# Kernel optimization log

Hardware: AMD Instinct MI355X
Metric: run time of the kernel (lower is better)

The kernel has to match this reference:

```python
import jax, jax.numpy as jnp
import numpy as np

B, L, D = 4, 2048, 64
N_HEAD = 4
LOCALITY = 0.2
PI = 3.141592653589793


def setup_inputs() -> dict:
    key = jax.random.key(0)
    k1, k2, k3 = jax.random.split(key, 3)
    mesh = jax.random.uniform(k1, (B, L, 2), dtype=jnp.float32)
    inputs = jax.random.normal(k2, (B, L, D), dtype=jnp.float32)
    lmda = jax.random.uniform(k3, (N_HEAD, 1, 1), dtype=jnp.float32)
    return {"mesh": mesh, "inputs": inputs, "lmda": lmda}


def reference(mesh, inputs, lmda):
    FMAX = jnp.finfo(jnp.float32).max
    # pairwise squared distances: (B, L, L)
    diff = mesh[:, :, None, :] - mesh[:, None, :, :]
    m_dist = jnp.sum(diff * diff, axis=-1)
    # per-head scale in (0, inf): tan(pi/4 * (1-eps) * (1 + sin(lmda)))
    scale = jnp.tan(0.25 * PI * (1.0 - 1e-07) * (1.0 + jnp.sin(lmda)))  # (H,1,1)
    scaled = m_dist[:, None, :, :] * scale  # (B, H, L, L)
    # row-wise quantile threshold (linear interpolation, matching torch.quantile)
    thresh = jnp.quantile(scaled, LOCALITY, axis=-1, keepdims=True)  # (B,H,L,1)
    masked = jnp.where(scaled <= thresh, scaled, FMAX)
    att = jax.nn.softmax(-masked, axis=-1)  # (B, H, L, L)
    # aggregate: (B,H,L,L) x (B,L,D) -> (B,L,H,D) -> (B,L,H*D)
    conv = jnp.einsum('bhnj,bjd->bnhd', att, inputs)
    conv = conv.reshape(inputs.shape[0], -1, N_HEAD * inputs.shape[-1])
    return jnp.concatenate([inputs, conv], axis=-1)
```

## Files before the change

kernel.cpp:

```cpp
#include <hip/hip_runtime.h>
#include <math.h>

#ifndef M_PI
#define M_PI 3.14159265358979323846
#endif

namespace {
constexpr int B_ = 4;
constexpr int L_ = 2048;
constexpr int D_ = 64;
constexpr int H_ = 4;
constexpr int RB = 8;
constexpr int KT = 64;
constexpr int NTILE = L_ / KT;
constexpr int CAPC = 256;
constexpr int OUTW = D_ + H_ * D_;
constexpr int APS = 2064;
}

typedef __attribute__((ext_vector_type(8))) short bf16x8;
typedef __attribute__((ext_vector_type(4))) float f32x4;

__device__ __forceinline__ unsigned bf16_rne(float x) {
    unsigned u = __float_as_uint(x);
    return (u + 0x7fffu + ((u >> 16) & 1u)) >> 16;
}

#define LDS_FENCE() __builtin_amdgcn_s_waitcnt(0xC07F)

__global__ __launch_bounds__(256) void prep_kernel(const float* __restrict__ inputs,
                                                   char* __restrict__ ws) {
    const int blk = blockIdx.x;
    const int b = blk >> 6;
    const int r6 = blk & 63;
    const int tile = r6 >> 2;
    const int qr = r6 & 3;
    const int t = threadIdx.x;
    const float* inb = inputs + ((size_t)b * L_ + tile * 128) * D_;
    char* wsb = ws + (size_t)b * (L_ * D_ * 2) + tile * (128 * D_ * 2);
    #pragma unroll
    for (int i = 0; i < 4; ++i) {
        const int idx = qr * 1024 + i * 256 + t;
        const int n  = idx & 63;
        const int kp = idx >> 6;
        const int kl = kp << 1;
        const float x0 = inb[kl * D_ + n];
        const float x1 = inb[(kl + 1) * D_ + n];
        const unsigned a = bf16_rne(x0);
        const unsigned c = bf16_rne(x1);
        const int chunk = (kl >> 3) * 64 + n;
        const int e = kl & 7;
        *reinterpret_cast<unsigned*>(wsb + chunk * 16 + e * 2) = a | (c << 16);
    }
}

__global__ __launch_bounds__(512, 8) void posatt_kernel(
    const float* __restrict__ mesh,
    const float* __restrict__ inputs,
    const float* __restrict__ lmda,
    const char* __restrict__ ws,
    float* __restrict__ out)
{
    __shared__ __align__(16) float2 s_mesh[L_];
    __shared__ __align__(16) char s_u1[16448];
    __shared__ float s_scale[H_];
    __shared__ float s_th[RB][H_];
    __shared__ float s_d409[RB], s_d410[RB];
    __shared__ float s_wsum[RB][H_];
    __shared__ unsigned s_ccw[8];

    const int t = threadIdx.x;
    const int l = t & 63;
    const int w = t >> 6;
    const int blk = blockIdx.x;
    const int b = blk >> 8;
    const int n0 = (blk & 255) * RB;

    if (t < H_) {
        const double lam = (double)lmda[t];
        const float C = (float)(0.25 * M_PI * (1.0 - 1e-07));
        const float s1 = (float)sin(lam);
        const float arg = __fmul_rn(C, __fadd_rn(1.0f, s1));
        s_scale[t] = (float)tan((double)arg);
    }
    {
        const float4* mg = reinterpret_cast<const float4*>(mesh + (size_t)b * L_ * 2);
        float4* msd = reinterpret_cast<float4*>(s_mesh);
        msd[t] = mg[t];
        msd[t + 512] = mg[t + 512];
    }
    __syncthreads();

    {
        unsigned* hw = reinterpret_cast<unsigned*>(s_u1) + w * 256;
        float* cw = reinterpret_cast<float*>(s_u1 + 8192) + w * CAPC;
        const int rl = w;
        const float2 me = s_mesh[n0 + rl];
        *reinterpret_cast<uint4*>(&hw[l * 4]) = make_uint4(0u, 0u, 0u, 0u);
        if (l == 0) s_ccw[w] = 0u;
        LDS_FENCE();
        #pragma unroll 4
        for (int it = 0; it < 32; ++it) {
            const int j = (it << 6) + l;
            const float2 mj = s_mesh[j];
            const float dx = __fsub_rn(me.x, mj.x);
            const float dy = __fsub_rn(me.y, mj.y);
            const float d = __fadd_rn(__fmul_rn(dx, dx), __fmul_rn(dy, dy));
            int bin = (int)(d * 128.0f); bin = bin < 255 ? bin : 255;
            atomicAdd(&hw[bin], 1u);
        }
        LDS_FENCE();
        const uint4 hv = *reinterpret_cast<const uint4*>(&hw[l * 4]);
        const unsigned p0 = hv.x, p1 = p0 + hv.y, p2 = p1 + hv.z, p3 = p2 + hv.w;
        unsigned sc = p3;
        #pragma unroll
        for (int off = 1; off < 64; off <<= 1) {
            const unsigned uu = __shfl_up(sc, off);
            if (l >= off) sc += uu;
        }
        const unsigned eb = sc - p3;
        const unsigned cum[4] = {eb + p0, eb + p1, eb + p2, eb + p3};
        int flo = -1, fhi = -1; unsigned fbase = 0u;
        #pragma unroll
        for (int e = 0; e < 4; ++e) {
            const unsigned prev = e ? cum[e - 1] : eb;
            if (cum[e] > 409u && prev <= 409u) { flo = l * 4 + e; fbase = prev; }
            if (cum[e] > 410u && prev <= 410u) { fhi = l * 4 + e; }
        }
        const unsigned long long bmlo = __ballot(flo >= 0);
        const int srclo = (int)__builtin_ctzll(bmlo);
        const int lo = __shfl(flo, srclo);
        const unsigned base = __shfl(fbase, srclo);
        const unsigned long long bmhi = __ballot(fhi >= 0);
        const int hi = __shfl(fhi, (int)__builtin_ctzll(bmhi));
        #pragma unroll 4
        for (int it = 0; it < 32; ++it) {
            const int j = (it << 6) + l;
            const float2 mj = s_mesh[j];
            const float dx = __fsub_rn(me.x, mj.x);
            const float dy = __fsub_rn(me.y, mj.y);
            const float d = __fadd_rn(__fmul_rn(dx, dx), __fmul_rn(dy, dy));
            int bin = (int)(d * 128.0f); bin = bin < 255 ? bin : 255;
            if (bin >= lo && bin <= hi) {
                const unsigned p = atomicAdd(&s_ccw[w], 1u);
                if (p < (unsigned)CAPC) cw[p] = d;
            }
        }
        LDS_FENCE();
        const int m = (int)min(s_ccw[w], (unsigned)CAPC);
        const int k409 = 409 - (int)base;
        const int k410 = 410 - (int)base;
        #pragma unroll 1
        for (int cc0 = 0; cc0 < m; cc0 += 64) {
            const int ci = cc0 + l;
            const float v = (ci < m) ? cw[ci] : 0.0f;
            int lt = 0, le = 0;
            #pragma unroll 8
            for (int i = 0; i < m; ++i) {
                const float u = cw[i];
                lt += (u < v) ? 1 : 0;
                le += (u <= v) ? 1 : 0;
            }
            if (ci < m) {
                if (lt <= k409 && k409 < le) s_d409[rl] = v;
                if (lt <= k410 && k410 < le) s_d410[rl] = v;
            }
        }
    }
    __syncthreads();

    if (t < RB * H_) {
        const int r = t >> 2, h = t & 3;
        const float scl = s_scale[h];
        const float s409 = __fmul_rn(s_d409[r], scl);
        const float s410 = __fmul_rn(s_d410[r], scl);
        const float pos = 0.2f * 2047.0f;
        const float g = pos - 409.0f;
        const float lw = 1.0f - g;
        s_th[r][h] = __fadd_rn(__fmul_rn(s409, lw), __fmul_rn(s410, g));
    }
    __syncthreads();

    const int mr   = t >> 4;
    const int h_b  = mr >> 3;
    const int r_b  = mr & 7;
    const int jg   = t & 15;
    const int row16 = ((h_b & 1) << 3) + r_b;
    const int pln   = h_b >> 1;
    const float2 me_b = s_mesh[n0 + r_b];
    const float sc_b = s_scale[h_b];
    const float th_b = s_th[r_b][h_b];
    const int ks4q_w = jg >> 1;
    const int chunk_w = ks4q_w * 16 + row16;
    const int chunkSw_w = chunk_w ^ (ks4q_w & 7);
    const int aoff = pln * APS + (chunkSw_w << 4) + ((jg & 1) << 3);
    float wacc = 0.0f;

    const int p_w  = w >> 2;
    const int ks_w = (w >> 1) & 1;
    const int nqh  = w & 1;
    const int ks4q_r = ks_w * 4 + (l >> 4);
    const int chunk_r = ks4q_r * 16 + (l & 15);
    const int aroff = p_w * APS + ((chunk_r ^ (ks4q_r & 7)) << 4);
    f32x4 acc[2];
    acc[0] = (f32x4)0.0f; acc[1] = (f32x4)0.0f;

    const float* inpb = inputs + (size_t)b * L_ * D_;
    const char* wsb = ws + (size_t)b * (L_ * D_ * 2);
    char* Abase = s_u1;
    char* Bbase = s_u1 + 2 * APS;

    #pragma unroll 1
    for (int tile = 0; tile < NTILE; ++tile) {
        __syncthreads();
        const uint4 bg = *reinterpret_cast<const uint4*>(wsb + ((size_t)(tile * 512 + t) << 4));
        const int k0 = tile * KT;
        {
            const float4 mq0 = *reinterpret_cast<const float4*>(&s_mesh[k0 + jg * 4]);
            const float4 mq1 = *reinterpret_cast<const float4*>(&s_mesh[k0 + jg * 4 + 2]);
            const float dx0 = __fsub_rn(me_b.x, mq0.x);
            const float dy0 = __fsub_rn(me_b.y, mq0.y);
            const float d0 = __fadd_rn(__fmul_rn(dx0, dx0), __fmul_rn(dy0, dy0));
            const float dx1 = __fsub_rn(me_b.x, mq0.z);
            const float dy1 = __fsub_rn(me_b.y, mq0.w);
            const float d1 = __fadd_rn(__fmul_rn(dx1, dx1), __fmul_rn(dy1, dy1));
            const float dx2 = __fsub_rn(me_b.x, mq1.x);
            const float dy2 = __fsub_rn(me_b.y, mq1.y);
            const float d2 = __fadd_rn(__fmul_rn(dx2, dx2), __fmul_rn(dy2, dy2));
            const float dx3 = __fsub_rn(me_b.x, mq1.z);
            const float dy3 = __fsub_rn(me_b.y, mq1.w);
            const float d3 = __fadd_rn(__fmul_rn(dx3, dx3), __fmul_rn(dy3, dy3));
            const float x0 = __fmul_rn(d0, sc_b);
            const float x1 = __fmul_rn(d1, sc_b);
            const float x2 = __fmul_rn(d2, sc_b);
            const float x3 = __fmul_rn(d3, sc_b);
            const float w0 = (x0 <= th_b) ? __expf(-x0) : 0.0f;
            const float w1 = (x1 <= th_b) ? __expf(-x1) : 0.0f;
            const float w2 = (x2 <= th_b) ? __expf(-x2) : 0.0f;
            const float w3 = (x3 <= th_b) ? __expf(-x3) : 0.0f;
            wacc += (w0 + w1) + (w2 + w3);
            const unsigned u01 = bf16_rne(w0) | (bf16_rne(w1) << 16);
            const unsigned u23 = bf16_rne(w2) | (bf16_rne(w3) << 16);
            *reinterpret_cast<uint2*>(Abase + aoff) = make_uint2(u01, u23);
        }
        *reinterpret_cast<uint4*>(Bbase + t * 16) = bg;
        __syncthreads();
        const bf16x8 afr = *reinterpret_cast<const bf16x8*>(Abase + aroff);
        #pragma unroll
        for (int i = 0; i < 2; ++i) {
            const int nq = nqh * 2 + i;
            const bf16x8 bfr = *reinterpret_cast<const bf16x8*>(
                Bbase + (((ks_w * 4 + (l >> 4)) * 64 + nq * 16 + (l & 15)) << 4));
            acc[i] = __builtin_amdgcn_mfma_f32_16x16x32_bf16(afr, bfr, acc[i], 0, 0, 0);
        }
    }
    __syncthreads();

    wacc += __shfl_xor(wacc, 1);
    wacc += __shfl_xor(wacc, 2);
    wacc += __shfl_xor(wacc, 4);
    wacc += __shfl_xor(wacc, 8);
    if ((l & 15) == 0) s_wsum[r_b][h_b] = wacc;
    {
        float4* Cz = reinterpret_cast<float4*>(s_u1);
        Cz[t] = make_float4(0.f, 0.f, 0.f, 0.f);
    }
    __syncthreads();
    {
        float* Cf = reinterpret_cast<float*>(s_u1);
        #pragma unroll
        for (int i = 0; i < 2; ++i) {
            const int nq = nqh * 2 + i;
            #pragma unroll
            for (int reg = 0; reg < 4; ++reg) {
                const int row = (l >> 4) * 4 + reg;
                const int col = nq * 16 + (l & 15);
                atomicAdd(&Cf[(p_w * 16 + row) * 64 + col], acc[i][reg]);
            }
        }
    }
    __syncthreads();
    {
        const float* Cf = reinterpret_cast<const float*>(s_u1);
        const int pr = t >> 4;
        const int p = pr >> 4;
        const int row16o = pr & 15;
        const int h = p * 2 + (row16o >> 3);
        const int r = row16o & 7;
        const int col = (t & 15) << 2;
        const float wsv = s_wsum[r][h];
        const float inv = (wsv != 0.0f) ? 1.0f / wsv : 0.0f;
        float4 r0 = *reinterpret_cast<const float4*>(&Cf[pr * 64 + col]);
        r0.x *= inv; r0.y *= inv; r0.z *= inv; r0.w *= inv;
        float* op = out + (size_t)(b * L_ + n0 + r) * OUTW + D_ + h * 64 + col;
        *reinterpret_cast<float4*>(op) = r0;
    }
    {
        const int r = t >> 6;
        const int c = t & 63;
        out[(size_t)(b * L_ + n0 + r) * OUTW + c] = inpb[(size_t)(n0 + r) * D_ + c];
    }
}

extern "C" void kernel_launch(void* const* d_in, const int* in_sizes, int n_in,
                              void* d_out, int out_size, void* d_ws, size_t ws_size,
                              hipStream_t stream) {
    const float* mesh   = (const float*)d_in[0];
    const float* inputs = (const float*)d_in[1];
    const float* lmda   = (const float*)d_in[2];
    float* out = (float*)d_out;
    char* ws = (char*)d_ws;
    (void)in_sizes; (void)n_in; (void)out_size; (void)ws_size;
    hipLaunchKernelGGL(prep_kernel, dim3(256), dim3(256), 0, stream, inputs, ws);
    hipLaunchKernelGGL(posatt_kernel, dim3(B_ * (L_ / RB)), dim3(512), 0, stream,
                       mesh, inputs, lmda, ws, out);
}
```

Before: 133.0 us.

## Add second-level histogram refinement for quantile and read mesh from global memory

```diff
diff --git a/kernel.cpp b/kernel.cpp
--- a/kernel.cpp
+++ b/kernel.cpp
@@ -61,7 +61,6 @@
     const char* __restrict__ ws,
     float* __restrict__ out)
 {
-    __shared__ __align__(16) float2 s_mesh[L_];
     __shared__ __align__(16) char s_u1[16448];
     __shared__ float s_scale[H_];
     __shared__ float s_th[RB][H_];
@@ -76,6 +75,8 @@
     const int b = blk >> 8;
     const int n0 = (blk & 255) * RB;
 
+    const float2* meshg = reinterpret_cast<const float2*>(mesh) + (size_t)b * L_;
+
     if (t < H_) {
         const double lam = (double)lmda[t];
         const float C = (float)(0.25 * M_PI * (1.0 - 1e-07));
@@ -83,26 +84,20 @@
         const float arg = __fmul_rn(C, __fadd_rn(1.0f, s1));
         s_scale[t] = (float)tan((double)arg);
     }
-    {
-        const float4* mg = reinterpret_cast<const float4*>(mesh + (size_t)b * L_ * 2);
-        float4* msd = reinterpret_cast<float4*>(s_mesh);
-        msd[t] = mg[t];
-        msd[t + 512] = mg[t + 512];
-    }
     __syncthreads();
 
     {
         unsigned* hw = reinterpret_cast<unsigned*>(s_u1) + w * 256;
         float* cw = reinterpret_cast<float*>(s_u1 + 8192) + w * CAPC;
         const int rl = w;
-        const float2 me = s_mesh[n0 + rl];
+        const float2 me = meshg[n0 + rl];
         *reinterpret_cast<uint4*>(&hw[l * 4]) = make_uint4(0u, 0u, 0u, 0u);
         if (l == 0) s_ccw[w] = 0u;
         LDS_FENCE();
         #pragma unroll 4
         for (int it = 0; it < 32; ++it) {
             const int j = (it << 6) + l;
-            const float2 mj = s_mesh[j];
+            const float2 mj = meshg[j];
             const float dx = __fsub_rn(me.x, mj.x);
             const float dy = __fsub_rn(me.y, mj.y);
             const float d = __fadd_rn(__fmul_rn(dx, dx), __fmul_rn(dy, dy));
@@ -110,33 +105,36 @@
             atomicAdd(&hw[bin], 1u);
         }
         LDS_FENCE();
-        const uint4 hv = *reinterpret_cast<const uint4*>(&hw[l * 4]);
-        const unsigned p0 = hv.x, p1 = p0 + hv.y, p2 = p1 + hv.z, p3 = p2 + hv.w;
-        unsigned sc = p3;
-        #pragma unroll
-        for (int off = 1; off < 64; off <<= 1) {
-            const unsigned uu = __shfl_up(sc, off);
-            if (l >= off) sc += uu;
-        }
-        const unsigned eb = sc - p3;
-        const unsigned cum[4] = {eb + p0, eb + p1, eb + p2, eb + p3};
-        int flo = -1, fhi = -1; unsigned fbase = 0u;
-        #pragma unroll
-        for (int e = 0; e < 4; ++e) {
-            const unsigned prev = e ? cum[e - 1] : eb;
-            if (cum[e] > 409u && prev <= 409u) { flo = l * 4 + e; fbase = prev; }
-            if (cum[e] > 410u && prev <= 410u) { fhi = l * 4 + e; }
-        }
-        const unsigned long long bmlo = __ballot(flo >= 0);
-        const int srclo = (int)__builtin_ctzll(bmlo);
-        const int lo = __shfl(flo, srclo);
-        const unsigned base = __shfl(fbase, srclo);
-        const unsigned long long bmhi = __ballot(fhi >= 0);
-        const int hi = __shfl(fhi, (int)__builtin_ctzll(bmhi));
+        int lo, hi; unsigned base;
+        {
+            const uint4 hv = *reinterpret_cast<const uint4*>(&hw[l * 4]);
+            const unsigned p0 = hv.x, p1 = p0 + hv.y, p2 = p1 + hv.z, p3 = p2 + hv.w;
+            unsigned sc = p3;
+            #pragma unroll
+            for (int off = 1; off < 64; off <<= 1) {
+                const unsigned uu = __shfl_up(sc, off);
+                if (l >= off) sc += uu;
+            }
+            const unsigned eb = sc - p3;
+            const unsigned cum[4] = {eb + p0, eb + p1, eb + p2, eb + p3};
+            int flo = -1, fhi = -1; unsigned fbase = 0u;
+            #pragma unroll
+            for (int e = 0; e < 4; ++e) {
+                const unsigned prev = e ? cum[e - 1] : eb;
+                if (cum[e] > 409u && prev <= 409u) { flo = l * 4 + e; fbase = prev; }
+                if (cum[e] > 410u && prev <= 410u) { fhi = l * 4 + e; }
+            }
+            const unsigned long long bmlo = __ballot(flo >= 0);
+            const int srclo = (int)__builtin_ctzll(bmlo);
+            lo = __shfl(flo, srclo);
+            base = __shfl(fbase, srclo);
+            const unsigned long long bmhi = __ballot(fhi >= 0);
+            hi = __shfl(fhi, (int)__builtin_ctzll(bmhi));
+        }
         #pragma unroll 4
         for (int it = 0; it < 32; ++it) {
             const int j = (it << 6) + l;
-            const float2 mj = s_mesh[j];
+            const float2 mj = meshg[j];
             const float dx = __fsub_rn(me.x, mj.x);
             const float dy = __fsub_rn(me.y, mj.y);
             const float d = __fadd_rn(__fmul_rn(dx, dx), __fmul_rn(dy, dy));
@@ -148,22 +146,77 @@
         }
         LDS_FENCE();
         const int m = (int)min(s_ccw[w], (unsigned)CAPC);
-        const int k409 = 409 - (int)base;
-        const int k410 = 410 - (int)base;
+        const unsigned k409 = 409u - base;
+        const unsigned k410 = 410u - base;
+        const float lo_edge = (float)lo * 0.0078125f;
+        const float sc2 = 32768.0f / (float)(hi - lo + 1);
+        *reinterpret_cast<uint4*>(&hw[l * 4]) = make_uint4(0u, 0u, 0u, 0u);
+        LDS_FENCE();
+        #pragma unroll 2
+        for (int ci = l; ci < m; ci += 64) {
+            const float v = cw[ci];
+            int b2 = (int)(__fmul_rn(__fsub_rn(v, lo_edge), sc2));
+            b2 = b2 < 255 ? b2 : 255; b2 = b2 > 0 ? b2 : 0;
+            atomicAdd(&hw[b2], 1u);
+        }
+        LDS_FENCE();
+        int lo2, hi2; unsigned base2;
+        {
+            const uint4 hv = *reinterpret_cast<const uint4*>(&hw[l * 4]);
+            const unsigned p0 = hv.x, p1 = p0 + hv.y, p2 = p1 + hv.z, p3 = p2 + hv.w;
+            unsigned sc = p3;
+            #pragma unroll
+            for (int off = 1; off < 64; off <<= 1) {
+                const unsigned uu = __shfl_up(sc, off);
+                if (l >= off) sc += uu;
+            }
+            const unsigned eb = sc - p3;
+            const unsigned cum[4] = {eb + p0, eb + p1, eb + p2, eb + p3};
+            int flo = -1, fhi = -1; unsigned fbase = 0u;
+            #pragma unroll
+            for (int e = 0; e < 4; ++e) {
+                const unsigned prev = e ? cum[e - 1] : eb;
+                if (cum[e] > k409 && prev <= k409) { flo = l * 4 + e; fbase = prev; }
+                if (cum[e] > k410 && prev <= k410) { fhi = l * 4 + e; }
+            }
+            const unsigned long long bmlo = __ballot(flo >= 0);
+            const int srclo = (int)__builtin_ctzll(bmlo);
+            lo2 = __shfl(flo, srclo);
+            base2 = __shfl(fbase, srclo);
+            const unsigned long long bmhi = __ballot(fhi >= 0);
+            hi2 = __shfl(fhi, (int)__builtin_ctzll(bmhi));
+        }
+        if (l == 0) s_ccw[w] = 0u;
+        LDS_FENCE();
+        float* c2 = reinterpret_cast<float*>(hw);
+        #pragma unroll 2
+        for (int ci = l; ci < m; ci += 64) {
+            const float v = cw[ci];
+            int b2 = (int)(__fmul_rn(__fsub_rn(v, lo_edge), sc2));
+            b2 = b2 < 255 ? b2 : 255; b2 = b2 > 0 ? b2 : 0;
+            if (b2 >= lo2 && b2 <= hi2) {
+                const unsigned p = atomicAdd(&s_ccw[w], 1u);
+                if (p < 256u) c2[p] = v;
+            }
+        }
+        LDS_FENCE();
+        const int c = (int)min(s_ccw[w], 256u);
+        const int q409 = (int)(k409 - base2);
+        const int q410 = (int)(k410 - base2);
         #pragma unroll 1
-        for (int cc0 = 0; cc0 < m; cc0 += 64) {
+        for (int cc0 = 0; cc0 < c; cc0 += 64) {
             const int ci = cc0 + l;
-            const float v = (ci < m) ? cw[ci] : 0.0f;
+            const float v = (ci < c) ? c2[ci] : 0.0f;
             int lt = 0, le = 0;
-            #pragma unroll 8
-            for (int i = 0; i < m; ++i) {
-                const float u = cw[i];
+            #pragma unroll 4
+            for (int i = 0; i < c; ++i) {
+                const float u = c2[i];
                 lt += (u < v) ? 1 : 0;
                 le += (u <= v) ? 1 : 0;
             }
-            if (ci < m) {
-                if (lt <= k409 && k409 < le) s_d409[rl] = v;
-                if (lt <= k410 && k410 < le) s_d410[rl] = v;
+            if (ci < c) {
+                if (lt <= q409 && q409 < le) s_d409[rl] = v;
+                if (lt <= q410 && q410 < le) s_d410[rl] = v;
             }
         }
     }
@@ -187,7 +240,7 @@
     const int jg   = t & 15;
     const int row16 = ((h_b & 1) << 3) + r_b;
     const int pln   = h_b >> 1;
-    const float2 me_b = s_mesh[n0 + r_b];
+    const float2 me_b = meshg[n0 + r_b];
     const float sc_b = s_scale[h_b];
     const float th_b = s_th[r_b][h_b];
     const int ks4q_w = jg >> 1;
@@ -216,8 +269,8 @@
         const uint4 bg = *reinterpret_cast<const uint4*>(wsb + ((size_t)(tile * 512 + t) << 4));
         const int k0 = tile * KT;
         {
-            const float4 mq0 = *reinterpret_cast<const float4*>(&s_mesh[k0 + jg * 4]);
-            const float4 mq1 = *reinterpret_cast<const float4*>(&s_mesh[k0 + jg * 4 + 2]);
+            const float4 mq0 = *reinterpret_cast<const float4*>(&meshg[k0 + jg * 4]);
+            const float4 mq1 = *reinterpret_cast<const float4*>(&meshg[k0 + jg * 4 + 2]);
             const float dx0 = __fsub_rn(me_b.x, mq0.x);
             const float dy0 = __fsub_rn(me_b.y, mq0.y);
             const float d0 = __fadd_rn(__fmul_rn(dx0, dx0), __fmul_rn(dy0, dy0));
```

Measured after the change: 137.1 us. 3.1% more time.
